# Kernel optimization log

Hardware: AMD Instinct MI355X
Metric: run time of the kernel (lower is better)

The kernel has to match this reference:

```python
import jax, jax.numpy as jnp
import numpy as np

HIDDEN = 2048
NUM_HEADS = 16
NUM_KV_HEADS = 4
HEAD_DIM = HIDDEN // NUM_HEADS  # 128
GROUP = NUM_HEADS // NUM_KV_HEADS  # 4
SCALE = HEAD_DIM ** -0.5


def setup_inputs() -> dict:
    key = jax.random.key(0)
    ks = jax.random.split(key, 9)
    B, S = 2, 2048
    kv_dim = HEAD_DIM * NUM_KV_HEADS
    std = HIDDEN ** -0.5
    return {
        "x": jax.random.normal(ks[0], (B, S, HIDDEN), dtype=jnp.float32),
        "Wq": jax.random.normal(ks[1], (HIDDEN, HIDDEN), dtype=jnp.float32) * std,
        "bq": jnp.zeros((HIDDEN,), dtype=jnp.float32),
        "Wk": jax.random.normal(ks[2], (HIDDEN, kv_dim), dtype=jnp.float32) * std,
        "bk": jnp.zeros((kv_dim,), dtype=jnp.float32),
        "Wv": jax.random.normal(ks[3], (HIDDEN, kv_dim), dtype=jnp.float32) * std,
        "bv": jnp.zeros((kv_dim,), dtype=jnp.float32),
        "Wo": jax.random.normal(ks[4], (HIDDEN, HIDDEN), dtype=jnp.float32) * std,
        "bo": jnp.zeros((HIDDEN,), dtype=jnp.float32),
    }


def reference(x, Wq, bq, Wk, bk, Wv, bv, Wo, bo):
    B, S, _ = x.shape
    # projections
    q = (x @ Wq + bq).reshape(B, S, NUM_KV_HEADS, GROUP, HEAD_DIM)  # grouped query heads
    k = (x @ Wk + bk).reshape(B, S, NUM_KV_HEADS, HEAD_DIM)
    v = (x @ Wv + bv).reshape(B, S, NUM_KV_HEADS, HEAD_DIM)
    # scores: [B, Hkv, G, Sq, Sk] -- same math as repeat_interleave of K/V over G,
    # but K/V are broadcast over the group axis instead of materialized.
    attn = jnp.einsum("bqhgd,bkhd->bhgqk", q, k) * SCALE
    attn = jax.nn.softmax(attn, axis=-1)
    out = jnp.einsum("bhgqk,bkhd->bqhgd", attn, v).reshape(B, S, HIDDEN)
    return out @ Wo + bo
```

## Files before the change

kernel.cpp:

```cpp
#include <hip/hip_runtime.h>


#define SEQ    2048
#define HIDDEN 2048

typedef __attribute__((ext_vector_type(8))) short v8s;
typedef __attribute__((ext_vector_type(4))) float v4f;

#define MFMA16(a,b,c) __builtin_amdgcn_mfma_f32_16x16x32_bf16((a),(b),(c),0,0,0)

__device__ __forceinline__ ushort f2b(float f){
  unsigned u = __float_as_uint(f);
  u += 0x7fffu + ((u >> 16) & 1u);
  return (ushort)(u >> 16);
}

__device__ __forceinline__ unsigned cvt_pk_bf16(float lo, float hi){
  unsigned r;
  asm("v_cvt_pk_bf16_f32 %0, %1, %2" : "=v"(r) : "v"(lo), "v"(hi));
  return r;
}

__device__ __forceinline__ void gload16(const void* g, void* l){
  __builtin_amdgcn_global_load_lds((const __attribute__((address_space(1))) void*)g,
                                   (__attribute__((address_space(3))) void*)l, 16, 0, 0);
}

#define WAIT_VM0   0x0F70
#define WAIT_LGKM0 0xC07F

__global__ void k_conv(const float* __restrict__ in, ushort* __restrict__ out, int n){
  int i = (blockIdx.x*256 + threadIdx.x)*4;
  if (i >= n) return;
  float4 f = *(const float4*)(in + i);
  ushort4 u; u.x=f2b(f.x); u.y=f2b(f.y); u.z=f2b(f.z); u.w=f2b(f.w);
  *(ushort4*)(out + i) = u;
}

__global__ void k_tconv(const float* __restrict__ in, ushort* __restrict__ out,
                        int rows, int cols){
  __shared__ float t[32][33];
  int tx = threadIdx.x & 31, ty = threadIdx.x >> 5;
  int c0 = blockIdx.x*32, r0 = blockIdx.y*32;
#pragma unroll
  for (int i=0;i<4;i++) t[ty+i*8][tx] = in[(size_t)(r0+ty+i*8)*cols + c0+tx];
  __syncthreads();
#pragma unroll
  for (int i=0;i<4;i++) out[(size_t)(c0+ty+i*8)*rows + r0+tx] = f2b(t[tx][ty+i*8]);
}

__global__ void k_tv(const ushort* __restrict__ vb, ushort* __restrict__ vT){
  __shared__ ushort t[32][33];
  int tx = threadIdx.x & 31, ty = threadIdx.x >> 5;
  int s0 = blockIdx.x*32, d0 = blockIdx.y*32, bh = blockIdx.z;
  int b = bh >> 2, h = bh & 3;
  const ushort* src = vb + (size_t)b*SEQ*512 + h*128;
#pragma unroll
  for (int i=0;i<4;i++) t[ty+i*8][tx] = src[(size_t)(s0+ty+i*8)*512 + d0+tx];
  __syncthreads();
  ushort* dst = vT + (size_t)bh*128*SEQ;
#pragma unroll
  for (int i=0;i<4;i++) dst[(size_t)(d0+ty+i*8)*SEQ + s0+tx] = t[tx][ty+i*8];
}

#define GEMM_MAIN(A_, Bt_, K_)                                                        \
  __shared__ ushort sA[128*32], sB[128*32];                                           \
  const int tid = threadIdx.x, lane = tid & 63, wid = tid >> 6;                       \
  const int wm = wid >> 1, wn = wid & 1, lm = lane & 15, q8 = (lane >> 4)*8;          \
  const int rowB = blockIdx.y*128, colB = blockIdx.x*128;                             \
  v4f acc[4][4] = {};                                                                 \
  for (int k0 = 0; k0 < (K_); k0 += 32){                                              \
    _Pragma("unroll")                                                                 \
    for (int it=0; it<2; it++){                                                       \
      int c = tid + it*256;                                                           \
      gload16((A_)  + (size_t)(rowB + (c>>2))*(K_) + k0 + (c&3)*8, (char*)sA + c*16); \
      gload16((Bt_) + (size_t)(colB + (c>>2))*(K_) + k0 + (c&3)*8, (char*)sB + c*16); \
    }                                                                                 \
    __syncthreads();                                                                  \
    v8s af[4], bfr[4];                                                                \
    _Pragma("unroll")                                                                 \
    for (int i=0;i<4;i++){                                                            \
      af[i]  = *(const v8s*)(sA + (wm*64 + i*16 + lm)*32 + q8);                       \
      bfr[i] = *(const v8s*)(sB + (wn*64 + i*16 + lm)*32 + q8);                       \
    }                                                                                 \
    _Pragma("unroll")                                                                 \
    for (int i=0;i<4;i++)                                                             \
      _Pragma("unroll")                                                               \
      for (int j=0;j<4;j++) acc[i][j] = MFMA16(af[i], bfr[j], acc[i][j]);             \
    __syncthreads();                                                                  \
  }                                                                                   \
  const int quad = lane >> 4;

__global__ __launch_bounds__(256) void k_gemm_qkv(
    const ushort* __restrict__ A, const ushort* __restrict__ Bt,
    const float* __restrict__ bq, const float* __restrict__ bk, const float* __restrict__ bv,
    ushort* __restrict__ qb, ushort* __restrict__ kb, ushort* __restrict__ vb){
  GEMM_MAIN(A, Bt, HIDDEN)
#pragma unroll
  for (int i=0;i<4;i++)
#pragma unroll
  for (int j=0;j<4;j++){
    int col = colB + wn*64 + j*16 + lm;
#pragma unroll
    for (int r=0;r<4;r++){
      int row = rowB + wm*64 + i*16 + quad*4 + r;
      float v = acc[i][j][r];
      if (col < 2048)      qb[(size_t)row*2048 + col]        = f2b(v + bq[col]);
      else if (col < 2560) kb[(size_t)row*512 + (col-2048)]  = f2b(v + bk[col-2048]);
      else                 vb[(size_t)row*512 + (col-2560)]  = f2b(v + bv[col-2560]);
    }
  }
}

__global__ __launch_bounds__(256) void k_gemm_out(
    const ushort* __restrict__ A, const ushort* __restrict__ Bt,
    const float* __restrict__ bo, float* __restrict__ out){
  GEMM_MAIN(A, Bt, HIDDEN)
#pragma unroll
  for (int i=0;i<4;i++)
#pragma unroll
  for (int j=0;j<4;j++){
    int col = colB + wn*64 + j*16 + lm;
#pragma unroll
    for (int r=0;r<4;r++){
      int row = rowB + wm*64 + i*16 + quad*4 + r;
      out[(size_t)row*2048 + col] = acc[i][j][r] + bo[col];
    }
  }
}

__global__ __launch_bounds__(512, 2) void k_attn(
    const ushort* __restrict__ qb, const ushort* __restrict__ kb,
    const ushort* __restrict__ vT, ushort* __restrict__ Ob){
  __shared__ ushort sK[2][64*128];
  __shared__ ushort sV[2][128*64];
  __shared__ ushort sP[8][1024];
  const int tid = threadIdx.x, lane = tid & 63, w = tid >> 6;
  const int lm = lane & 15, quad = lane >> 4, q8 = quad*8;
  const int pair = blockIdx.x & 7;
  const int hkv = pair & 3, b = pair >> 2;
  const int qt = (blockIdx.x >> 3) & 15, g = blockIdx.x >> 7;
  const int head = hkv*4 + g;
  const float C = 0.08838834764831845f * 1.4426950408889634f;

  const ushort* kbb = kb + (size_t)b*SEQ*512 + hkv*128;
  const ushort* vbb = vT + (size_t)(b*4+hkv)*128*SEQ;

  const int kk = lane >> 4, ksw = lane & 15;
  const int dd = lane >> 3, vsw = lane & 7;

#define STAGE_K(t, buf) { _Pragma("unroll") for (int i=0;i<2;i++){                     \
    int c = w*2 + i; int key = c*4 + kk; int wd = ksw ^ (key & 15);                    \
    gload16(kbb + (size_t)((t)*64 + key)*512 + wd*8, &sK[buf][c*512 + lane*8]); } }
#define STAGE_V(t, buf) { _Pragma("unroll") for (int i=0;i<2;i++){                     \
    int c = w*2 + i; int drow = c*8 + dd; int wd = vsw ^ dd;                           \
    gload16(vbb + (size_t)drow*SEQ + (t)*64 + wd*8, &sV[buf][c*512 + lane*8]); } }

  v8s qf[4];
#pragma unroll
  for (int ks=0; ks<4; ks++)
    qf[ks] = *(const v8s*)(qb + (size_t)(b*SEQ + qt*128 + w*16 + lm)*HIDDEN
                              + head*128 + ks*32 + q8);

  v4f o[8] = {};
  float lreg = 0.f;

  STAGE_K(0, 0)
  STAGE_V(0, 0)
  __builtin_amdgcn_s_waitcnt(WAIT_VM0);
  __syncthreads();

  for (int t=0; t<32; t++){
    const int cur = t & 1;
    if (t < 31) STAGE_K(t+1, cur^1)

    v4f sacc[4] = {};
#pragma unroll
    for (int ks=0; ks<4; ks++){
      v8s kf[4];
#pragma unroll
      for (int kt=0; kt<4; kt++)
        kf[kt] = *(const v8s*)(&sK[cur][(kt*16+lm)*128 + ((ks*4+quad)^lm)*8]);
      __builtin_amdgcn_s_setprio(1);
#pragma unroll
      for (int kt=0; kt<4; kt++)
        sacc[kt] = MFMA16(kf[kt], qf[ks], sacc[kt]);
      __builtin_amdgcn_s_setprio(0);
    }

    {
      float rs = 0.f;
#pragma unroll
      for (int kt=0; kt<4; kt++){
        float p0 = __builtin_amdgcn_exp2f(sacc[kt][0]*C);
        float p1 = __builtin_amdgcn_exp2f(sacc[kt][1]*C);
        float p2 = __builtin_amdgcn_exp2f(sacc[kt][2]*C);
        float p3 = __builtin_amdgcn_exp2f(sacc[kt][3]*C);
        rs += (p0+p1)+(p2+p3);
        uint2 pk;
        pk.x = cvt_pk_bf16(p0, p1);
        pk.y = cvt_pk_bf16(p2, p3);
        int kc = kt >> 1;
        int dl = ((kt&1)*2 + (quad>>1))*16 + lm;
        *(uint2*)(&sP[w][kc*512 + dl*8 + (quad&1)*4]) = pk;
      }
      lreg += rs;
    }

    __builtin_amdgcn_s_waitcnt(WAIT_VM0);
    __syncthreads();
    if (t < 31) STAGE_V(t+1, cur^1)

    __builtin_amdgcn_s_waitcnt(WAIT_LGKM0);
    v8s pa[2];
#pragma unroll
    for (int kc=0; kc<2; kc++)
      pa[kc] = *(const v8s*)(&sP[w][kc*512 + lane*8]);
#pragma unroll
    for (int kc=0; kc<2; kc++){
      v8s vf[8];
#pragma unroll
      for (int dt=0; dt<8; dt++)
        vf[dt] = *(const v8s*)(&sV[cur][(dt*16+lm)*64 + ((kc*4+quad)^(lm&7))*8]);
      __builtin_amdgcn_s_setprio(1);
#pragma unroll
      for (int dt=0; dt<8; dt++)
        o[dt] = MFMA16(pa[kc], vf[dt], o[dt]);
      __builtin_amdgcn_s_setprio(0);
    }
  }

  {
    float lv = lreg;
    lv += __shfl_xor(lv, 16);
    lv += __shfl_xor(lv, 32);
    float inv[4];
#pragma unroll
    for (int r=0;r<4;r++) inv[r] = 1.0f / __shfl(lv, (lane & 48) + quad*4 + r);
#pragma unroll
    for (int dt=0; dt<8; dt++)
#pragma unroll
      for (int r=0;r<4;r++){
        int row = b*SEQ + qt*128 + w*16 + quad*4 + r;
        int col = head*128 + dt*16 + lm;
        Ob[(size_t)row*HIDDEN + col] = f2b(o[dt][r]*inv[r]);
      }
  }
#undef STAGE_K
#undef STAGE_V
}

extern "C" void kernel_launch(void* const* d_in, const int* in_sizes, int n_in,
                              void* d_out, int out_size, void* d_ws, size_t ws_size,
                              hipStream_t stream){
  const float* x  = (const float*)d_in[0];
  const float* Wq = (const float*)d_in[1];
  const float* bq = (const float*)d_in[2];
  const float* Wk = (const float*)d_in[3];
  const float* bk = (const float*)d_in[4];
  const float* Wv = (const float*)d_in[5];
  const float* bv = (const float*)d_in[6];
  const float* Wo = (const float*)d_in[7];
  const float* bo = (const float*)d_in[8];
  float* out = (float*)d_out;

  ushort* xb  = (ushort*)d_ws;
  ushort* Wt  = xb  + 8388608;
  ushort* Wto = Wt  + 6291456;
  ushort* qb  = Wto + 4194304;
  ushort* kb  = qb  + 8388608;
  ushort* vb  = kb  + 2097152;
  ushort* vT  = vb  + 2097152;
  ushort* Ob  = vT  + 2097152;

  k_conv <<<8192, 256, 0, stream>>>(x, xb, 8388608);
  k_tconv<<<dim3(64,64), 256, 0, stream>>>(Wq, Wt, 2048, 2048);
  k_tconv<<<dim3(16,64), 256, 0, stream>>>(Wk, Wt + 4194304, 2048, 512);
  k_tconv<<<dim3(16,64), 256, 0, stream>>>(Wv, Wt + 5242880, 2048, 512);
  k_tconv<<<dim3(64,64), 256, 0, stream>>>(Wo, Wto, 2048, 2048);
  k_gemm_qkv<<<dim3(24,32), 256, 0, stream>>>(xb, Wt, bq, bk, bv, qb, kb, vb);
  k_tv  <<<dim3(64,4,8), 256, 0, stream>>>(vb, vT);
  k_attn<<<512, 512, 0, stream>>>(qb, kb, vT, Ob);
  k_gemm_out<<<dim3(16,32), 256, 0, stream>>>(Ob, Wto, bo, out);
}
```

Measured before the change: 329.7 us.

## Rewrite projection GEMMs as 256x256 double-buffered, swizzled 8-wave pipeline

Replaces the simple 128x128 single-buffered GEMM (K-step 32, two barriers per step) with a 256x256 tile, K-step 64, 512-thread kernel. It double-buffers LDS with an XOR swizzle and interleaves global-to-LDS prefetch of the next tiles between four MFMA phases, using setprio and sched barriers. The aim is more operand reuse per LDS byte, fewer bank conflicts and hidden global latency. The cost is far fewer blocks: 192 for QKV and 128 for the output GEMM, which can underfill the 256 CUs, plus large register and LDS use.

```diff
diff --git a/kernel.cpp b/kernel.cpp
--- a/kernel.cpp
+++ b/kernel.cpp
@@ -27,6 +27,7 @@
 }
 
 #define WAIT_VM0   0x0F70
+#define WAIT_VM2   0x0F72
 #define WAIT_LGKM0 0xC07F
 
 __global__ void k_conv(const float* __restrict__ in, ushort* __restrict__ out, int n){
@@ -63,47 +64,110 @@
   for (int i=0;i<4;i++) dst[(size_t)(d0+ty+i*8)*SEQ + s0+tx] = t[tx][ty+i*8];
 }
 
-#define GEMM_MAIN(A_, Bt_, K_)                                                        \
-  __shared__ ushort sA[128*32], sB[128*32];                                           \
-  const int tid = threadIdx.x, lane = tid & 63, wid = tid >> 6;                       \
-  const int wm = wid >> 1, wn = wid & 1, lm = lane & 15, q8 = (lane >> 4)*8;          \
-  const int rowB = blockIdx.y*128, colB = blockIdx.x*128;                             \
-  v4f acc[4][4] = {};                                                                 \
-  for (int k0 = 0; k0 < (K_); k0 += 32){                                              \
-    _Pragma("unroll")                                                                 \
-    for (int it=0; it<2; it++){                                                       \
-      int c = tid + it*256;                                                           \
-      gload16((A_)  + (size_t)(rowB + (c>>2))*(K_) + k0 + (c&3)*8, (char*)sA + c*16); \
-      gload16((Bt_) + (size_t)(colB + (c>>2))*(K_) + k0 + (c&3)*8, (char*)sB + c*16); \
-    }                                                                                 \
-    __syncthreads();                                                                  \
-    v8s af[4], bfr[4];                                                                \
-    _Pragma("unroll")                                                                 \
-    for (int i=0;i<4;i++){                                                            \
-      af[i]  = *(const v8s*)(sA + (wm*64 + i*16 + lm)*32 + q8);                       \
-      bfr[i] = *(const v8s*)(sB + (wn*64 + i*16 + lm)*32 + q8);                       \
-    }                                                                                 \
-    _Pragma("unroll")                                                                 \
-    for (int i=0;i<4;i++)                                                             \
-      _Pragma("unroll")                                                               \
-      for (int j=0;j<4;j++) acc[i][j] = MFMA16(af[i], bfr[j], acc[i][j]);             \
-    __syncthreads();                                                                  \
-  }                                                                                   \
-  const int quad = lane >> 4;
-
-__global__ __launch_bounds__(256) void k_gemm_qkv(
+#define GEMM256_MAIN(A_, Bt_)                                                          \
+  __shared__ ushort sA[2][2][128*64], sB[2][2][128*64];                                \
+  const int tid = threadIdx.x, lane = tid & 63, w = tid >> 6;                          \
+  const int wm = w >> 2, wn = w & 3, lm = lane & 15, quad = lane >> 4;                 \
+  const int wh = wn >> 1, wl = wn & 1, l3 = lane >> 3, l7m = lm & 7;                   \
+  const int swz = ((lane & 7) ^ (l3 & 7)) * 8;                                         \
+  const int rowB = blockIdx.y*256, colB = blockIdx.x*256;                              \
+  const ushort* Ag = (A_); const ushort* Bg = (Bt_);                                   \
+  v4f acc[8][4] = {};                                                                  \
+  STG_A(0,0,0) STG_A(0,1,0) STG_B(0,0,0) STG_B(0,1,0) STG_A(1,0,1)                     \
+  __builtin_amdgcn_s_waitcnt(WAIT_VM2);                                                \
+  __builtin_amdgcn_s_barrier(); __builtin_amdgcn_sched_barrier(0);                     \
+  for (int t = 0; t < 32; t++){                                                        \
+    const int p = t & 1, pn = p ^ 1;                                                   \
+    const int tn  = (t+1 < 32) ? t+1 : t;                                              \
+    const int tnn = (t+2 < 32) ? t+2 : 31;                                             \
+    v8s a0[4][2], a1[4][2], bb0[2][2], bb1[2][2];                                      \
+                                                                              \
+    _Pragma("unroll")                                                                  \
+    for (int i=0;i<4;i++){ LDA(a0[i][0], i, 0) LDA(a0[i][1], i, 1) }                   \
+    _Pragma("unroll")                                                                  \
+    for (int j=0;j<2;j++){ LDB(bb0[j][0], j, 0) LDB(bb0[j][1], j, 1) }                 \
+    STG_A(tn, 1, pn)                                                                   \
+    __builtin_amdgcn_s_barrier(); __builtin_amdgcn_sched_barrier(0);                   \
+    __builtin_amdgcn_s_waitcnt(WAIT_LGKM0); __builtin_amdgcn_sched_barrier(0);         \
+    __builtin_amdgcn_s_setprio(1);                                                     \
+    _Pragma("unroll")                                                                  \
+    for (int ks=0;ks<2;ks++)                                                           \
+      _Pragma("unroll")                                                                \
+      for (int i=0;i<4;i++)                                                            \
+        _Pragma("unroll")                                                              \
+        for (int j=0;j<2;j++) acc[i][j] = MFMA16(a0[i][ks], bb0[j][ks], acc[i][j]);    \
+    __builtin_amdgcn_s_setprio(0);                                                     \
+    __builtin_amdgcn_s_barrier(); __builtin_amdgcn_sched_barrier(0);                   \
+                                                                              \
+    _Pragma("unroll")                                                                  \
+    for (int j=0;j<2;j++){ LDB(bb1[j][0], j+2, 0) LDB(bb1[j][1], j+2, 1) }             \
+    STG_B(tn, 0, pn)                                                                   \
+    __builtin_amdgcn_s_barrier(); __builtin_amdgcn_sched_barrier(0);                   \
+    __builtin_amdgcn_s_waitcnt(WAIT_LGKM0); __builtin_amdgcn_sched_barrier(0);         \
+    __builtin_amdgcn_s_setprio(1);                                                     \
+    _Pragma("unroll")                                                                  \
+    for (int ks=0;ks<2;ks++)                                                           \
+      _Pragma("unroll")                                                                \
+      for (int i=0;i<4;i++)                                                            \
+        _Pragma("unroll")                                                              \
+        for (int j=0;j<2;j++) acc[i][j+2] = MFMA16(a0[i][ks], bb1[j][ks], acc[i][j+2]);\
+    __builtin_amdgcn_s_setprio(0);                                                     \
+    __builtin_amdgcn_s_barrier(); __builtin_amdgcn_sched_barrier(0);                   \
+                                                                              \
+    _Pragma("unroll")                                                                  \
+    for (int i=0;i<4;i++){ LDA(a1[i][0], i+4, 0) LDA(a1[i][1], i+4, 1) }               \
+    STG_B(tn, 1, pn)                                                                   \
+    __builtin_amdgcn_s_barrier(); __builtin_amdgcn_sched_barrier(0);                   \
+    __builtin_amdgcn_s_waitcnt(WAIT_LGKM0); __builtin_amdgcn_sched_barrier(0);         \
+    __builtin_amdgcn_s_setprio(1);                                                     \
+    _Pragma("unroll")                                                                  \
+    for (int ks=0;ks<2;ks++)                                                           \
+      _Pragma("unroll")                                                                \
+      for (int i=0;i<4;i++)                                                            \
+        _Pragma("unroll")                                                              \
+        for (int j=0;j<2;j++) acc[i+4][j] = MFMA16(a1[i][ks], bb0[j][ks], acc[i+4][j]);\
+    __builtin_amdgcn_s_setprio(0);                                                     \
+    __builtin_amdgcn_s_barrier(); __builtin_amdgcn_sched_barrier(0);                   \
+                  \
+    STG_A(tnn, 0, p)                                                                   \
+    __builtin_amdgcn_s_waitcnt(WAIT_VM2); __builtin_amdgcn_sched_barrier(0);           \
+    __builtin_amdgcn_s_barrier(); __builtin_amdgcn_sched_barrier(0);                   \
+    __builtin_amdgcn_s_setprio(1);                                                     \
+    _Pragma("unroll")                                                                  \
+    for (int ks=0;ks<2;ks++)                                                           \
+      _Pragma("unroll")                                                                \
+      for (int i=0;i<4;i++)                                                            \
+        _Pragma("unroll")                                                              \
+        for (int j=0;j<2;j++)                                                          \
+          acc[i+4][j+2] = MFMA16(a1[i][ks], bb1[j][ks], acc[i+4][j+2]);                \
+    __builtin_amdgcn_s_setprio(0);                                                     \
+    __builtin_amdgcn_s_barrier(); __builtin_amdgcn_sched_barrier(0);                   \
+  }
+
+#define STG_A(t_, h_, buf_) { _Pragma("unroll") for (int i_=0;i_<2;i_++){              \
+    int c_ = w*2 + i_;                                                                 \
+    gload16(Ag + (size_t)(rowB + (h_)*128 + c_*8 + l3)*HIDDEN + (t_)*64 + swz,         \
+            &sA[buf_][h_][c_*512 + lane*8]); } }
+#define STG_B(t_, h_, buf_) { _Pragma("unroll") for (int i_=0;i_<2;i_++){              \
+    int c_ = w*2 + i_;                                                                 \
+    gload16(Bg + (size_t)(colB + (h_)*128 + c_*8 + l3)*HIDDEN + (t_)*64 + swz,         \
+            &sB[buf_][h_][c_*512 + lane*8]); } }
+#define LDA(dst_, i_, ks_) dst_ = *(const v8s*)(&sA[p][wm][((i_)*16+lm)*64 + ((((ks_)*4+quad))^l7m)*8]);
+#define LDB(dst_, j_, ks_) dst_ = *(const v8s*)(&sB[p][wh][(wl*64 + (j_)*16+lm)*64 + ((((ks_)*4+quad))^l7m)*8]);
+
+__global__ __launch_bounds__(512, 1) void k_gemm_qkv(
     const ushort* __restrict__ A, const ushort* __restrict__ Bt,
     const float* __restrict__ bq, const float* __restrict__ bk, const float* __restrict__ bv,
     ushort* __restrict__ qb, ushort* __restrict__ kb, ushort* __restrict__ vb){
-  GEMM_MAIN(A, Bt, HIDDEN)
-#pragma unroll
-  for (int i=0;i<4;i++)
+  GEMM256_MAIN(A, Bt)
+#pragma unroll
+  for (int i=0;i<8;i++)
 #pragma unroll
   for (int j=0;j<4;j++){
     int col = colB + wn*64 + j*16 + lm;
 #pragma unroll
     for (int r=0;r<4;r++){
-      int row = rowB + wm*64 + i*16 + quad*4 + r;
+      int row = rowB + wm*128 + i*16 + quad*4 + r;
       float v = acc[i][j][r];
       if (col < 2048)      qb[(size_t)row*2048 + col]        = f2b(v + bq[col]);
       else if (col < 2560) kb[(size_t)row*512 + (col-2048)]  = f2b(v + bk[col-2048]);
@@ -112,18 +176,18 @@
   }
 }
 
-__global__ __launch_bounds__(256) void k_gemm_out(
+__global__ __launch_bounds__(512, 1) void k_gemm_out(
     const ushort* __restrict__ A, const ushort* __restrict__ Bt,
     const float* __restrict__ bo, float* __restrict__ out){
-  GEMM_MAIN(A, Bt, HIDDEN)
-#pragma unroll
-  for (int i=0;i<4;i++)
+  GEMM256_MAIN(A, Bt)
+#pragma unroll
+  for (int i=0;i<8;i++)
 #pragma unroll
   for (int j=0;j<4;j++){
     int col = colB + wn*64 + j*16 + lm;
 #pragma unroll
     for (int r=0;r<4;r++){
-      int row = rowB + wm*64 + i*16 + quad*4 + r;
+      int row = rowB + wm*128 + i*16 + quad*4 + r;
       out[(size_t)row*2048 + col] = acc[i][j][r] + bo[col];
     }
   }
@@ -278,8 +342,8 @@
   k_tconv<<<dim3(16,64), 256, 0, stream>>>(Wk, Wt + 4194304, 2048, 512);
   k_tconv<<<dim3(16,64), 256, 0, stream>>>(Wv, Wt + 5242880, 2048, 512);
   k_tconv<<<dim3(64,64), 256, 0, stream>>>(Wo, Wto, 2048, 2048);
-  k_gemm_qkv<<<dim3(24,32), 256, 0, stream>>>(xb, Wt, bq, bk, bv, qb, kb, vb);
+  k_gemm_qkv<<<dim3(12,16), 512, 0, stream>>>(xb, Wt, bq, bk, bv, qb, kb, vb);
   k_tv  <<<dim3(64,4,8), 256, 0, stream>>>(vb, vT);
   k_attn<<<512, 512, 0, stream>>>(qb, kb, vT, Ob);
-  k_gemm_out<<<dim3(16,32), 256, 0, stream>>>(Ob, Wto, bo, out);
-}
+  k_gemm_out<<<dim3(8,16), 512, 0, stream>>>(Ob, Wto, bo, out);
+}
```

Measured after the change: 348.2 us. +5.6%, slower.
